# Kernel optimization log

Hardware: AMD Instinct MI355X
Metric: run time of the kernel (lower is better)

Reference implementation:

```python
import jax, jax.numpy as jnp
import numpy as np
from jax import lax

EPS = 1e-8  # numerical safety in squash sqrt (torch repo uses plain sqrt)

def squash(s, axis=-1):
    sq = jnp.sum(s * s, axis=axis, keepdims=True)
    return (sq / (1.0 + sq)) * s / jnp.sqrt(sq + EPS)

def conv2d(x, w, b, stride):
    y = lax.conv_general_dilated(x, w, (stride, stride), 'VALID',
                                 dimension_numbers=('NCHW', 'OIHW', 'NCHW'))
    return y + b[None, :, None, None]

def setup_inputs() -> dict:
    key = jax.random.key(0)
    ks = jax.random.split(key, 12)
    B = 256
    x = jax.random.normal(ks[0], (B, 1, 28, 28), dtype=jnp.float32)
    conv_w = jax.random.normal(ks[1], (256, 1, 9, 9), dtype=jnp.float32) * 0.05
    conv_b = jnp.zeros((256,), dtype=jnp.float32)
    caps1_w = jax.random.normal(ks[2], (32, 8, 256, 9, 9), dtype=jnp.float32) * 0.01
    caps1_b = jnp.zeros((32, 8), dtype=jnp.float32)
    caps2_w = jax.random.normal(ks[3], (10, 1152, 8, 16), dtype=jnp.float32)  # torch.randn
    dec_w1 = jax.random.normal(ks[4], (160, 512), dtype=jnp.float32) * 0.05
    dec_b1 = jnp.zeros((512,), dtype=jnp.float32)
    dec_w2 = jax.random.normal(ks[5], (512, 1024), dtype=jnp.float32) * 0.04
    dec_b2 = jnp.zeros((1024,), dtype=jnp.float32)
    dec_w3 = jax.random.normal(ks[6], (1024, 784), dtype=jnp.float32) * 0.03
    dec_b3 = jnp.zeros((784,), dtype=jnp.float32)
    return {"x": x, "conv_w": conv_w, "conv_b": conv_b, "caps1_w": caps1_w,
            "caps1_b": caps1_b, "caps2_w": caps2_w, "dec_w1": dec_w1,
            "dec_b1": dec_b1, "dec_w2": dec_w2, "dec_b2": dec_b2,
            "dec_w3": dec_w3, "dec_b3": dec_b3}

def reference(x, conv_w, conv_b, caps1_w, caps1_b, caps2_w,
              dec_w1, dec_b1, dec_w2, dec_b2, dec_w3, dec_b3):
    B = x.shape[0]
    # conv + relu -> [B,256,20,20]
    h = jax.nn.relu(conv2d(x, conv_w, conv_b, 1))
    # CapsLayerOne: 32 parallel convs folded into one grouped-out conv -> [B,256,6,6]
    u = conv2d(h, caps1_w.reshape(32 * 8, 256, 9, 9), caps1_b.reshape(-1), 2)
    u = u.reshape(B, 32, 8, 6, 6)                    # [B,caps,ch,h,w]
    # replicate torch cat(dim=-1).view(B,8,-1): flatten order (h, caps, w) per channel
    u = u.transpose(0, 2, 3, 1, 4).reshape(B, 8, 1152)  # [B,8,N]
    u = squash(u.transpose(0, 2, 1))                 # [B,N,8], N=1152
    # CapsLayerTwo dynamic routing
    x_hat = jnp.einsum('bni,cnio->cbno', u, caps2_w)[:, :, :, None, :]  # [10,B,N,1,16]
    b = jnp.zeros_like(x_hat)
    v = None
    for i in range(3):
        c = jax.nn.softmax(b, axis=2)
        s = jnp.sum(x_hat * c, axis=2, keepdims=True)  # [10,B,1,1,16]
        v = squash(s)
        if i != 2:
            b = b + jnp.sum(x_hat * v, axis=-1, keepdims=True)
    v = v[:, :, 0, 0, :].transpose(1, 0, 2)            # [B,10,16]
    class_scores = jnp.sqrt(jnp.sum(v * v, axis=-1) + EPS)  # [B,10]
    class_probabilities = jax.nn.softmax(class_scores, axis=-1)
    labels = jnp.argmax(class_probabilities, axis=1)
    y = jax.nn.one_hot(labels, 10, dtype=v.dtype)
    masked = (v * y[:, :, None]).reshape(B, 160)
    d = jax.nn.relu(masked @ dec_w1 + dec_b1)
    d = jax.nn.relu(d @ dec_w2 + dec_b2)
    reconstructions = jax.nn.sigmoid(d @ dec_w3 + dec_b3)  # [B,784]
    return (class_probabilities, reconstructions)
```

## Files before the change

kernel.cpp:

```cpp
#include <hip/hip_runtime.h>
#include <cstdint>
#include <cstddef>

#define EPSF 1e-8f

typedef __attribute__((ext_vector_type(8))) short bf16x8;
typedef __attribute__((ext_vector_type(4))) float f32x4;
typedef unsigned short ushort_t;

static __device__ __forceinline__ ushort_t f2bf(float f) {
  unsigned u = __builtin_bit_cast(unsigned, f);
  unsigned r = (u + 0x7FFFu + ((u >> 16) & 1u)) >> 16;
  return (ushort_t)r;
}
static __device__ __forceinline__ float bf2f(ushort_t h) {
  return __builtin_bit_cast(float, (unsigned)h << 16);
}

__global__ __launch_bounds__(256) void conv1_kernel(
    const float* __restrict__ x, const float* __restrict__ cw,
    const float* __restrict__ cb, ushort_t* __restrict__ h2x)
{
  int oy = blockIdx.x, b = blockIdx.y, ci = threadIdx.x;
  float w[81];
#pragma unroll
  for (int i = 0; i < 81; ++i) w[i] = cw[ci * 81 + i];
  float bias = cb[ci];
  float acc[20];
#pragma unroll
  for (int ox = 0; ox < 20; ++ox) acc[ox] = bias;
  const float* xb = x + (size_t)b * 784;
  for (int ky = 0; ky < 9; ++ky) {
    const float* row = xb + (oy + ky) * 28;
    float rv[28];
#pragma unroll
    for (int c = 0; c < 28; ++c) rv[c] = row[c];
#pragma unroll
    for (int kx = 0; kx < 9; ++kx) {
      float wv = w[ky * 9 + kx];
#pragma unroll
      for (int ox = 0; ox < 20; ++ox)
        acc[ox] = fmaf(rv[ox + kx], wv, acc[ox]);
    }
  }
  int cblk = ci >> 5, jj = ci & 31;
#pragma unroll
  for (int ox = 0; ox < 20; ++ox) {
    float a = fmaxf(acc[ox], 0.f);
    ushort_t hi = f2bf(a);
    ushort_t lo = f2bf(a - bf2f(hi));
    size_t o = ((size_t)(oy * 20 + ox) * 256 + b) * 512 + cblk * 64 + jj;
    h2x[o] = hi; h2x[o + 32] = lo;
  }
}

__global__ __launch_bounds__(256) void w2k_prep_kernel(
    const float* __restrict__ c1w, ushort_t* __restrict__ w2k)
{
  int co = blockIdx.x, ci = threadIdx.x;
  const float* src = c1w + ((size_t)co * 256 + ci) * 81;
  int cblk = ci >> 5, jj = ci & 31;
  for (int tap = 0; tap < 81; ++tap) {
    float v = src[tap];
    ushort_t hi = f2bf(v);
    size_t dst = ((size_t)co * 81 + tap) * 512 + cblk * 64 + jj;
    w2k[dst] = hi;
    w2k[dst + 32] = f2bf(v - bf2f(hi));
  }
}

__global__ __launch_bounds__(256, 2) void caps1_mfma_kernel(
    const ushort_t* __restrict__ h2x, const ushort_t* __restrict__ w2k,
    float* __restrict__ partial)
{
  int bid = blockIdx.x;
  int ks = bid & 3;
  int nt = (bid >> 2) & 1;
  int kt = (bid >> 3) & 1;
  int mt = (bid >> 4) & 1;
  int pos = bid >> 5;
  int ys = pos / 6, xs = pos % 6;
  int t = threadIdx.x;
  int wid = t >> 6, lane = t & 63;
  int wr = wid >> 1, wc = wid & 1;
  int lrow = lane & 15, g = lane >> 4;

  int b0 = mt * 128, n0 = nt * 128;
  int tb    = kt ? 41 : 0;
  int ntaps = kt ? 40 : 41;
  int nht   = 2 * ntaps;

  __shared__ ushort_t lds[2][2][128 * 64];

  f32x4 acc[4][4];
#pragma unroll
  for (int i = 0; i < 4; ++i)
#pragma unroll
    for (int j = 0; j < 4; ++j) acc[i][j] = (f32x4){0.f, 0.f, 0.f, 0.f};

  int c_ = (t & 7) ^ ((t >> 3) & 7);
  size_t aRowB[4], bRow81[4];
  int ldsBase[4];
#pragma unroll
  for (int i = 0; i < 4; ++i) {
    int row = i * 32 + (t >> 3);
    aRowB[i]  = (size_t)(b0 + row) * 512 + ks * 128 + c_ * 8;
    bRow81[i] = (size_t)(n0 + row) * 81;
    ldsBase[i] = (i * 32 + wid * 8) * 64;
  }

  auto stage = [&](int j, int bufi) {
    int tap = tb + (j >> 1);
    int half = j & 1;
    int ky = tap / 9, kx = tap - ky * 9;
    int pix = (2 * ys + ky) * 20 + 2 * xs + kx;
    size_t apix = (size_t)pix * 131072 + half * 64;
    int sub = ks * 128 + half * 64 + c_ * 8;
#pragma unroll
    for (int i = 0; i < 4; ++i) {
      const ushort_t* ga = h2x + apix + aRowB[i];
      const ushort_t* gb = w2k + (bRow81[i] + tap) * 512 + sub;
      __builtin_amdgcn_global_load_lds(ga, &lds[bufi][0][ldsBase[i]], 16, 0, 0);
      __builtin_amdgcn_global_load_lds(gb, &lds[bufi][1][ldsBase[i]], 16, 0, 0);
    }
  };

  bf16x8 a_h[4], a_l[4], b_h[4], b_l[4];
  auto read_frags = [&](int bufi) {
    const ushort_t* LA = &lds[bufi][0][0];
    const ushort_t* LB = &lds[bufi][1][0];
#pragma unroll
    for (int f = 0; f < 4; ++f) {
      int ra = wr * 64 + f * 16 + lrow;
      int sa = ra * 64;
      a_h[f] = *(const bf16x8*)(LA + sa + ((g)     ^ (ra & 7)) * 8);
      a_l[f] = *(const bf16x8*)(LA + sa + ((4 + g) ^ (ra & 7)) * 8);
      int rb = wc * 64 + f * 16 + lrow;
      int sb = rb * 64;
      b_h[f] = *(const bf16x8*)(LB + sb + ((g)     ^ (rb & 7)) * 8);
      b_l[f] = *(const bf16x8*)(LB + sb + ((4 + g) ^ (rb & 7)) * 8);
    }
  };

  stage(0, 0);
  stage(1, 1);
  asm volatile("s_waitcnt vmcnt(8)" ::: "memory");
  __builtin_amdgcn_sched_barrier(0);
  __builtin_amdgcn_s_barrier();

  for (int j = 0; j < nht; ++j) {
    int cur = j & 1;
    read_frags(cur);
    asm volatile("s_waitcnt lgkmcnt(0)" ::: "memory");
    __builtin_amdgcn_sched_barrier(0);
    __builtin_amdgcn_s_barrier();

    if (j + 2 < nht) stage(j + 2, cur);
    __builtin_amdgcn_sched_barrier(0);

    __builtin_amdgcn_s_setprio(1);
#pragma unroll
    for (int mf = 0; mf < 4; ++mf)
#pragma unroll
      for (int nf = 0; nf < 4; ++nf) {
        acc[mf][nf] = __builtin_amdgcn_mfma_f32_16x16x32_bf16(a_h[mf], b_h[nf], acc[mf][nf], 0, 0, 0);
        acc[mf][nf] = __builtin_amdgcn_mfma_f32_16x16x32_bf16(a_h[mf], b_l[nf], acc[mf][nf], 0, 0, 0);
        acc[mf][nf] = __builtin_amdgcn_mfma_f32_16x16x32_bf16(a_l[mf], b_h[nf], acc[mf][nf], 0, 0, 0);
      }
    __builtin_amdgcn_s_setprio(0);
    __builtin_amdgcn_sched_barrier(0);

    if (j + 2 < nht) { asm volatile("s_waitcnt vmcnt(8)" ::: "memory"); }
    else             { asm volatile("s_waitcnt vmcnt(0)" ::: "memory"); }
    __builtin_amdgcn_sched_barrier(0);
    __builtin_amdgcn_s_barrier();
  }

  float* pp = partial + (size_t)(kt * 4 + ks) * 2359296;
#pragma unroll
  for (int mf = 0; mf < 4; ++mf) {
    int m = b0 + wr * 64 + mf * 16 + g * 4;
#pragma unroll
    for (int nf = 0; nf < 4; ++nf) {
      int n = n0 + wc * 64 + nf * 16 + lrow;
#pragma unroll
      for (int r = 0; r < 4; ++r)
        pp[((size_t)(pos * 256 + m + r)) * 256 + n] = acc[mf][nf][r];
    }
  }
}

__global__ __launch_bounds__(256) void combine_kernel(
    const float* __restrict__ partial, const float* __restrict__ c1b, float* __restrict__ u)
{
  int gidx = blockIdx.x * 256 + threadIdx.x;
  int caps = gidx & 31;
  int b = (gidx >> 5) & 255;
  int pos = gidx >> 13;
  int ys = pos / 6, xs = pos % 6;
  size_t base = ((size_t)pos * 256 + b) * 256 + caps * 8;
  f32x4 s0 = {0.f, 0.f, 0.f, 0.f}, s1 = {0.f, 0.f, 0.f, 0.f};
#pragma unroll
  for (int ksp = 0; ksp < 8; ++ksp) {
    const float* pp = partial + (size_t)ksp * 2359296 + base;
    s0 += *(const f32x4*)pp;
    s1 += *(const f32x4*)(pp + 4);
  }
  const float* bp = c1b + caps * 8;
#pragma unroll
  for (int i = 0; i < 4; ++i) { s0[i] += bp[i]; s1[i] += bp[4 + i]; }
  float sq = s0[0]*s0[0] + s0[1]*s0[1] + s0[2]*s0[2] + s0[3]*s0[3]
           + s1[0]*s1[0] + s1[1]*s1[1] + s1[2]*s1[2] + s1[3]*s1[3];
  float scale = sq / ((1.f + sq) * sqrtf(sq + EPSF));
  int nvec = ys * 192 + caps * 6 + xs;
  float* up = u + ((size_t)b * 1152 + nvec) * 8;
  f32x4 o0, o1;
#pragma unroll
  for (int i = 0; i < 4; ++i) { o0[i] = s0[i] * scale; o1[i] = s1[i] * scale; }
  *(f32x4*)up = o0;
  *(f32x4*)(up + 4) = o1;
}

__global__ __launch_bounds__(320) void xhat_kernel(
    const float* __restrict__ u, const float* __restrict__ W2, float* __restrict__ xh)
{
  int np = blockIdx.x;
  int t = threadIdx.x;
  int c  = t >> 5;
  int nh = (t >> 4) & 1;
  int o  = t & 15;
  int n = np * 2 + nh;
  __shared__ float us[2][256][8];
  for (int e = t; e < 4096; e += 320) {
    int b = e >> 4;
    int nn = (e >> 3) & 1, i = e & 7;
    us[nn][b][i] = u[((size_t)b * 1152 + np * 2 + nn) * 8 + i];
  }
  __syncthreads();
  float wcol[8];
  const float* wp = W2 + (((size_t)c * 1152 + n) * 8) * 16 + o;
#pragma unroll
  for (int i = 0; i < 8; ++i) wcol[i] = wp[i * 16];
  float* xp = xh + ((size_t)(c * 256) * 1152 + n) * 16 + o;
  for (int b = 0; b < 256; ++b) {
    float s = 0.f;
#pragma unroll
    for (int i = 0; i < 8; ++i) s = fmaf(us[nh][b][i], wcol[i], s);
    xp[(size_t)b * 1152 * 16] = s;
  }
}

__global__ __launch_bounds__(256) void routing_kernel(
    const float* __restrict__ xhat, float* __restrict__ vout)
{
  int b = blockIdx.x, c = blockIdx.y, t = threadIdx.x;
  int wid = t >> 6, lane = t & 63;
  float xh[5][16];
  float bn[5] = {0, 0, 0, 0, 0};
  bool valid[5];
  const float* xp = xhat + ((size_t)(c * 256 + b)) * 1152 * 16;
#pragma unroll
  for (int j = 0; j < 5; ++j) {
    int n = t + 256 * j;
    valid[j] = (n < 1152);
    if (valid[j]) {
      const f32x4* q = (const f32x4*)(xp + (size_t)n * 16);
#pragma unroll
      for (int v4 = 0; v4 < 4; ++v4) {
        f32x4 val = q[v4];
#pragma unroll
        for (int k = 0; k < 4; ++k) xh[j][v4 * 4 + k] = val[k];
      }
    } else {
#pragma unroll
      for (int o = 0; o < 16; ++o) xh[j][o] = 0.f;
    }
  }
  __shared__ float redm[4], redz[4], reds[64], sv[16];
  float scale = 0.f;
  for (int it = 0; it < 3; ++it) {
    float m = -1e30f;
#pragma unroll
    for (int j = 0; j < 5; ++j) if (valid[j]) m = fmaxf(m, bn[j]);
    for (int d = 1; d < 64; d <<= 1) m = fmaxf(m, __shfl_xor(m, d));
    if (lane == 0) redm[wid] = m;
    __syncthreads();
    m = fmaxf(fmaxf(redm[0], redm[1]), fmaxf(redm[2], redm[3]));
    float e[5]; float z = 0.f;
#pragma unroll
    for (int j = 0; j < 5; ++j) { e[j] = valid[j] ? expf(bn[j] - m) : 0.f; z += e[j]; }
    for (int d = 1; d < 64; d <<= 1) z += __shfl_xor(z, d);
    if (lane == 0) redz[wid] = z;
    __syncthreads();
    z = redz[0] + redz[1] + redz[2] + redz[3];
    float ps[16];
#pragma unroll
    for (int o = 0; o < 16; ++o) ps[o] = 0.f;
#pragma unroll
    for (int j = 0; j < 5; ++j)
#pragma unroll
      for (int o = 0; o < 16; ++o) ps[o] = fmaf(e[j], xh[j][o], ps[o]);
#pragma unroll
    for (int o = 0; o < 16; ++o) {
      float vv = ps[o];
      for (int d = 1; d < 64; d <<= 1) vv += __shfl_xor(vv, d);
      if (lane == 0) reds[wid * 16 + o] = vv;
    }
    __syncthreads();
    if (t < 16) sv[t] = (reds[t] + reds[16 + t] + reds[32 + t] + reds[48 + t]) / z;
    __syncthreads();
    float vsc[16]; float sq = 0.f;
#pragma unroll
    for (int o = 0; o < 16; ++o) { vsc[o] = sv[o]; sq += sv[o] * sv[o]; }
    scale = sq / ((1.f + sq) * sqrtf(sq + EPSF));
    if (it < 2) {
#pragma unroll
      for (int j = 0; j < 5; ++j) if (valid[j]) {
        float dot = 0.f;
#pragma unroll
        for (int o = 0; o < 16; ++o) dot = fmaf(xh[j][o], vsc[o] * scale, dot);
        bn[j] += dot;
      }
    }
    __syncthreads();
  }
  if (t < 16) vout[((size_t)c * 256 + b) * 16 + t] = sv[t] * scale;
}

__global__ __launch_bounds__(256) void classify_kernel(
    const float* __restrict__ v, float* __restrict__ probs, float* __restrict__ masked)
{
  int b = blockIdx.x, t = threadIdx.x;
  __shared__ float sc[10], vv[160];
  int c = t >> 4, o = t & 15;
  float val = 0.f;
  if (t < 160) { val = v[((size_t)c * 256 + b) * 16 + o]; vv[t] = val; }
  float sq = val * val;
  sq += __shfl_xor(sq, 1); sq += __shfl_xor(sq, 2);
  sq += __shfl_xor(sq, 4); sq += __shfl_xor(sq, 8);
  if (t < 160 && o == 0) sc[c] = sqrtf(sq + EPSF);
  __syncthreads();
  float m = sc[0];
#pragma unroll
  for (int i = 1; i < 10; ++i) m = fmaxf(m, sc[i]);
  float ee[10]; float Z = 0.f;
#pragma unroll
  for (int i = 0; i < 10; ++i) { ee[i] = expf(sc[i] - m); Z += ee[i]; }
  float p[10];
#pragma unroll
  for (int i = 0; i < 10; ++i) p[i] = ee[i] / Z;
  int label = 0; float best = p[0];
#pragma unroll
  for (int i = 1; i < 10; ++i) if (p[i] > best) { best = p[i]; label = i; }
  if (t < 10) probs[(size_t)b * 10 + t] = p[t];
  if (t < 160) masked[(size_t)b * 160 + t] = (c == label) ? vv[t] : 0.f;
}

template <int ACT>
__global__ __launch_bounds__(256) void mlp_kernel(
    const float* __restrict__ A, const float* __restrict__ W,
    const float* __restrict__ bias, float* __restrict__ C, int N, int K)
{
  int j = blockIdx.x * 64 + (threadIdx.x & 63);
  int ty = threadIdx.x >> 6;
  int m0 = blockIdx.y * 16;
  __shared__ float As[16][33];
  float acc[4] = {0.f, 0.f, 0.f, 0.f};
  for (int k0 = 0; k0 < K; k0 += 32) {
    for (int e = threadIdx.x; e < 512; e += 256) {
      int r = e >> 5, kk = e & 31;
      As[r][kk] = A[(size_t)(m0 + r) * K + k0 + kk];
    }
    __syncthreads();
    if (j < N) {
      for (int kk = 0; kk < 32; ++kk) {
        float wv = W[(size_t)(k0 + kk) * N + j];
#pragma unroll
        for (int r = 0; r < 4; ++r) acc[r] = fmaf(As[ty + 4 * r][kk], wv, acc[r]);
      }
    }
    __syncthreads();
  }
  if (j < N) {
    float bv = bias[j];
#pragma unroll
    for (int r = 0; r < 4; ++r) {
      float xx = acc[r] + bv;
      if (ACT == 0) xx = fmaxf(xx, 0.f);
      else xx = 1.f / (1.f + expf(-xx));
      C[(size_t)(m0 + ty + 4 * r) * N + j] = xx;
    }
  }
}

extern "C" void kernel_launch(void* const* d_in, const int* in_sizes, int n_in,
                              void* d_out, int out_size, void* d_ws, size_t ws_size,
                              hipStream_t stream)
{
  const float* x   = (const float*)d_in[0];
  const float* cw  = (const float*)d_in[1];
  const float* cb  = (const float*)d_in[2];
  const float* c1w = (const float*)d_in[3];
  const float* c1b = (const float*)d_in[4];
  const float* c2w = (const float*)d_in[5];
  const float* w1  = (const float*)d_in[6];
  const float* b1  = (const float*)d_in[7];
  const float* w2  = (const float*)d_in[8];
  const float* b2  = (const float*)d_in[9];
  const float* w3  = (const float*)d_in[10];
  const float* b3  = (const float*)d_in[11];
  float* out = (float*)d_out;

  char* p = (char*)d_ws;
  float* xh = (float*)p;
  ushort_t* h2x = (ushort_t*)p; p += (size_t)52428800 * 2;
  ushort_t* w2k = (ushort_t*)p; p += (size_t)10616832 * 2;
  float* partial = (float*)p;   p += (size_t)8 * 2359296 * 4;
  float* u       = (float*)p;   p += (size_t)2359296 * 4;
  float* v       = (float*)p;   p += (size_t)40960 * 4;
  float* masked  = (float*)p;   p += (size_t)40960 * 4;
  float* a1      = (float*)p;   p += (size_t)131072 * 4;
  float* a2      = (float*)p;   p += (size_t)262144 * 4;

  hipLaunchKernelGGL(w2k_prep_kernel, dim3(256), dim3(256), 0, stream, c1w, w2k);
  hipLaunchKernelGGL(conv1_kernel, dim3(20, 256), dim3(256), 0, stream, x, cw, cb, h2x);
  hipLaunchKernelGGL(caps1_mfma_kernel, dim3(1152), dim3(256), 0, stream, h2x, w2k, partial);
  hipLaunchKernelGGL(combine_kernel, dim3(1152), dim3(256), 0, stream, partial, c1b, u);
  hipLaunchKernelGGL(xhat_kernel, dim3(576), dim3(320), 0, stream, u, c2w, xh);
  hipLaunchKernelGGL(routing_kernel, dim3(256, 10), dim3(256), 0, stream, xh, v);
  hipLaunchKernelGGL(classify_kernel, dim3(256), dim3(256), 0, stream, v, out, masked);
  hipLaunchKernelGGL(mlp_kernel<0>, dim3(8, 16), dim3(256), 0, stream, masked, w1, b1, a1, 512, 160);
  hipLaunchKernelGGL(mlp_kernel<0>, dim3(16, 16), dim3(256), 0, stream, a1, w2, b2, a2, 1024, 512);
  hipLaunchKernelGGL(mlp_kernel<1>, dim3(13, 16), dim3(256), 0, stream, a2, w3, b3, out + 2560, 784, 1024);
}
```

Baseline: 585.4 us.

## Fuse x_hat computation into routing kernel and drop the xhat intermediate buffer

The separate xhat kernel, which wrote the 10x256x1152x16 float x_hat tensor (~189MB) to global memory, is removed. The routing kernel now computes each x_hat vector in registers from u and caps2_w directly. Block indices are remapped so consecutive blocks share the same batch element across classes, improving cache reuse of u and W2. This trades a large write and read of x_hat for redundant W2 reads per batch element, which should mostly hit in L2/MALL since W2 is about 5.9MB.

```diff
diff --git a/kernel.cpp b/kernel.cpp
--- a/kernel.cpp
+++ b/kernel.cpp
@@ -221,55 +221,42 @@
   *(f32x4*)(up + 4) = o1;
 }
 
-__global__ __launch_bounds__(320) void xhat_kernel(
-    const float* __restrict__ u, const float* __restrict__ W2, float* __restrict__ xh)
-{
-  int np = blockIdx.x;
+__global__ __launch_bounds__(256) void routing_kernel(
+    const float* __restrict__ u, const float* __restrict__ W2, float* __restrict__ vout)
+{
+  int bid = blockIdx.x;
+  int c, b;
+  if (bid < 2048) { c = bid & 7; b = bid >> 3; }
+  else { int r = bid - 2048; int x = r & 7; c = 8 + (x >> 2); b = (r >> 3) * 4 + (x & 3); }
   int t = threadIdx.x;
-  int c  = t >> 5;
-  int nh = (t >> 4) & 1;
-  int o  = t & 15;
-  int n = np * 2 + nh;
-  __shared__ float us[2][256][8];
-  for (int e = t; e < 4096; e += 320) {
-    int b = e >> 4;
-    int nn = (e >> 3) & 1, i = e & 7;
-    us[nn][b][i] = u[((size_t)b * 1152 + np * 2 + nn) * 8 + i];
-  }
-  __syncthreads();
-  float wcol[8];
-  const float* wp = W2 + (((size_t)c * 1152 + n) * 8) * 16 + o;
-#pragma unroll
-  for (int i = 0; i < 8; ++i) wcol[i] = wp[i * 16];
-  float* xp = xh + ((size_t)(c * 256) * 1152 + n) * 16 + o;
-  for (int b = 0; b < 256; ++b) {
-    float s = 0.f;
-#pragma unroll
-    for (int i = 0; i < 8; ++i) s = fmaf(us[nh][b][i], wcol[i], s);
-    xp[(size_t)b * 1152 * 16] = s;
-  }
-}
-
-__global__ __launch_bounds__(256) void routing_kernel(
-    const float* __restrict__ xhat, float* __restrict__ vout)
-{
-  int b = blockIdx.x, c = blockIdx.y, t = threadIdx.x;
   int wid = t >> 6, lane = t & 63;
   float xh[5][16];
   float bn[5] = {0, 0, 0, 0, 0};
   bool valid[5];
-  const float* xp = xhat + ((size_t)(c * 256 + b)) * 1152 * 16;
+  const float* ub = u + (size_t)b * 9216;
+  const float* Wc = W2 + (size_t)c * 147456;
 #pragma unroll
   for (int j = 0; j < 5; ++j) {
     int n = t + 256 * j;
     valid[j] = (n < 1152);
     if (valid[j]) {
-      const f32x4* q = (const f32x4*)(xp + (size_t)n * 16);
-#pragma unroll
-      for (int v4 = 0; v4 < 4; ++v4) {
-        f32x4 val = q[v4];
-#pragma unroll
-        for (int k = 0; k < 4; ++k) xh[j][v4 * 4 + k] = val[k];
+      float uv[8];
+      *(f32x4*)&uv[0] = *(const f32x4*)(ub + (size_t)n * 8);
+      *(f32x4*)&uv[4] = *(const f32x4*)(ub + (size_t)n * 8 + 4);
+      const float* wn = Wc + (size_t)n * 128;
+#pragma unroll
+      for (int oc = 0; oc < 4; ++oc) {
+        f32x4 a0 = {0.f, 0.f, 0.f, 0.f}, a1 = {0.f, 0.f, 0.f, 0.f};
+#pragma unroll
+        for (int i = 0; i < 4; ++i) {
+          f32x4 w0 = *(const f32x4*)(wn + (2 * i) * 16 + oc * 4);
+          f32x4 w1 = *(const f32x4*)(wn + (2 * i + 1) * 16 + oc * 4);
+          a0 += uv[2 * i] * w0;
+          a1 += uv[2 * i + 1] * w1;
+        }
+        f32x4 s = a0 + a1;
+#pragma unroll
+        for (int k = 0; k < 4; ++k) xh[j][oc * 4 + k] = s[k];
       }
     } else {
 #pragma unroll
@@ -412,7 +399,6 @@
   float* out = (float*)d_out;
 
   char* p = (char*)d_ws;
-  float* xh = (float*)p;
   ushort_t* h2x = (ushort_t*)p; p += (size_t)52428800 * 2;
   ushort_t* w2k = (ushort_t*)p; p += (size_t)10616832 * 2;
   float* partial = (float*)p;   p += (size_t)8 * 2359296 * 4;
@@ -426,8 +412,7 @@
   hipLaunchKernelGGL(conv1_kernel, dim3(20, 256), dim3(256), 0, stream, x, cw, cb, h2x);
   hipLaunchKernelGGL(caps1_mfma_kernel, dim3(1152), dim3(256), 0, stream, h2x, w2k, partial);
   hipLaunchKernelGGL(combine_kernel, dim3(1152), dim3(256), 0, stream, partial, c1b, u);
-  hipLaunchKernelGGL(xhat_kernel, dim3(576), dim3(320), 0, stream, u, c2w, xh);
-  hipLaunchKernelGGL(routing_kernel, dim3(256, 10), dim3(256), 0, stream, xh, v);
+  hipLaunchKernelGGL(routing_kernel, dim3(2560), dim3(256), 0, stream, u, c2w, v);
   hipLaunchKernelGGL(classify_kernel, dim3(256), dim3(256), 0, stream, v, out, masked);
   hipLaunchKernelGGL(mlp_kernel<0>, dim3(8, 16), dim3(256), 0, stream, masked, w1, b1, a1, 512, 160);
   hipLaunchKernelGGL(mlp_kernel<0>, dim3(16, 16), dim3(256), 0, stream, a1, w2, b2, a2, 1024, 512);
```

Result: slower. 797.2 us (+36.2%).

## Enlarge caps1 MFMA tile to 256x256 per block and store x_hat in bf16

Applied to the files above, without the earlier changes.

The caps1 GEMM now gives each 512-thread block the full 256x256 output tile. Previously it used 128x128 tiles over 1152 blocks, so this quadruples operand reuse per global/LDS load. It also splits the fragment reads and MFMA work into two halves so LDS reads overlap compute. Separately, x_hat is written and read as bf16 instead of fp32, halving traffic between xhat_kernel and routing_kernel at some precision cost. The grid drops to 288 blocks, which may underfill the 256 CUs, and the larger accumulator set raises register pressure.

```diff
diff --git a/kernel.cpp b/kernel.cpp
--- a/kernel.cpp
+++ b/kernel.cpp
@@ -69,44 +69,41 @@
   }
 }
 
-__global__ __launch_bounds__(256, 2) void caps1_mfma_kernel(
+__global__ __launch_bounds__(512, 2) void caps1_mfma_kernel(
     const ushort_t* __restrict__ h2x, const ushort_t* __restrict__ w2k,
     float* __restrict__ partial)
 {
   int bid = blockIdx.x;
   int ks = bid & 3;
-  int nt = (bid >> 2) & 1;
-  int kt = (bid >> 3) & 1;
-  int mt = (bid >> 4) & 1;
-  int pos = bid >> 5;
+  int kt = (bid >> 2) & 1;
+  int pos = bid >> 3;
   int ys = pos / 6, xs = pos % 6;
   int t = threadIdx.x;
   int wid = t >> 6, lane = t & 63;
-  int wr = wid >> 1, wc = wid & 1;
+  int wrow = wid >> 2, wcol = wid & 3;
   int lrow = lane & 15, g = lane >> 4;
 
-  int b0 = mt * 128, n0 = nt * 128;
   int tb    = kt ? 41 : 0;
   int ntaps = kt ? 40 : 41;
   int nht   = 2 * ntaps;
 
-  __shared__ ushort_t lds[2][2][128 * 64];
-
-  f32x4 acc[4][4];
-#pragma unroll
-  for (int i = 0; i < 4; ++i)
+  __shared__ ushort_t lds[2][2][256 * 64];
+
+  f32x4 acc[8][4];
+#pragma unroll
+  for (int i = 0; i < 8; ++i)
 #pragma unroll
     for (int j = 0; j < 4; ++j) acc[i][j] = (f32x4){0.f, 0.f, 0.f, 0.f};
 
   int c_ = (t & 7) ^ ((t >> 3) & 7);
-  size_t aRowB[4], bRow81[4];
-  int ldsBase[4];
+  size_t aRowB[4], bTap[4];
+  int ldsB[4];
 #pragma unroll
   for (int i = 0; i < 4; ++i) {
-    int row = i * 32 + (t >> 3);
-    aRowB[i]  = (size_t)(b0 + row) * 512 + ks * 128 + c_ * 8;
-    bRow81[i] = (size_t)(n0 + row) * 81;
-    ldsBase[i] = (i * 32 + wid * 8) * 64;
+    int row = i * 64 + (t >> 3);
+    aRowB[i] = (size_t)row * 512 + ks * 128 + c_ * 8;
+    bTap[i]  = (size_t)row * 81 * 512 + ks * 128 + c_ * 8;
+    ldsB[i]  = i * 4096 + wid * 512;
   }
 
   auto stage = [&](int j, int bufi) {
@@ -115,31 +112,46 @@
     int ky = tap / 9, kx = tap - ky * 9;
     int pix = (2 * ys + ky) * 20 + 2 * xs + kx;
     size_t apix = (size_t)pix * 131072 + half * 64;
-    int sub = ks * 128 + half * 64 + c_ * 8;
+    size_t boff = (size_t)tap * 512 + half * 64;
 #pragma unroll
     for (int i = 0; i < 4; ++i) {
-      const ushort_t* ga = h2x + apix + aRowB[i];
-      const ushort_t* gb = w2k + (bRow81[i] + tap) * 512 + sub;
-      __builtin_amdgcn_global_load_lds(ga, &lds[bufi][0][ldsBase[i]], 16, 0, 0);
-      __builtin_amdgcn_global_load_lds(gb, &lds[bufi][1][ldsBase[i]], 16, 0, 0);
+      __builtin_amdgcn_global_load_lds(h2x + apix + aRowB[i], &lds[bufi][0][ldsB[i]], 16, 0, 0);
+      __builtin_amdgcn_global_load_lds(w2k + bTap[i] + boff,  &lds[bufi][1][ldsB[i]], 16, 0, 0);
     }
   };
 
   bf16x8 a_h[4], a_l[4], b_h[4], b_l[4];
-  auto read_frags = [&](int bufi) {
+  auto readB = [&](int bufi) {
+    const ushort_t* LB = &lds[bufi][1][0];
+#pragma unroll
+    for (int nf = 0; nf < 4; ++nf) {
+      int rb = wcol * 64 + nf * 16 + lrow;
+      int sb = rb * 64;
+      b_h[nf] = *(const bf16x8*)(LB + sb + ((g)     ^ (rb & 7)) * 8);
+      b_l[nf] = *(const bf16x8*)(LB + sb + ((4 + g) ^ (rb & 7)) * 8);
+    }
+  };
+  auto readA = [&](int bufi, int hf) {
     const ushort_t* LA = &lds[bufi][0][0];
-    const ushort_t* LB = &lds[bufi][1][0];
-#pragma unroll
-    for (int f = 0; f < 4; ++f) {
-      int ra = wr * 64 + f * 16 + lrow;
+#pragma unroll
+    for (int mf = 0; mf < 4; ++mf) {
+      int ra = wrow * 128 + (hf * 4 + mf) * 16 + lrow;
       int sa = ra * 64;
-      a_h[f] = *(const bf16x8*)(LA + sa + ((g)     ^ (ra & 7)) * 8);
-      a_l[f] = *(const bf16x8*)(LA + sa + ((4 + g) ^ (ra & 7)) * 8);
-      int rb = wc * 64 + f * 16 + lrow;
-      int sb = rb * 64;
-      b_h[f] = *(const bf16x8*)(LB + sb + ((g)     ^ (rb & 7)) * 8);
-      b_l[f] = *(const bf16x8*)(LB + sb + ((4 + g) ^ (rb & 7)) * 8);
-    }
+      a_h[mf] = *(const bf16x8*)(LA + sa + ((g)     ^ (ra & 7)) * 8);
+      a_l[mf] = *(const bf16x8*)(LA + sa + ((4 + g) ^ (ra & 7)) * 8);
+    }
+  };
+  auto mfmaH = [&](int hf) {
+    __builtin_amdgcn_s_setprio(1);
+#pragma unroll
+    for (int mf = 0; mf < 4; ++mf)
+#pragma unroll
+      for (int nf = 0; nf < 4; ++nf) {
+        acc[hf * 4 + mf][nf] = __builtin_amdgcn_mfma_f32_16x16x32_bf16(a_h[mf], b_h[nf], acc[hf * 4 + mf][nf], 0, 0, 0);
+        acc[hf * 4 + mf][nf] = __builtin_amdgcn_mfma_f32_16x16x32_bf16(a_h[mf], b_l[nf], acc[hf * 4 + mf][nf], 0, 0, 0);
+        acc[hf * 4 + mf][nf] = __builtin_amdgcn_mfma_f32_16x16x32_bf16(a_l[mf], b_h[nf], acc[hf * 4 + mf][nf], 0, 0, 0);
+      }
+    __builtin_amdgcn_s_setprio(0);
   };
 
   stage(0, 0);
@@ -150,26 +162,18 @@
 
   for (int j = 0; j < nht; ++j) {
     int cur = j & 1;
-    read_frags(cur);
+    readB(cur);
+    readA(cur, 0);
+    asm volatile("s_waitcnt lgkmcnt(0)" ::: "memory");
+    __builtin_amdgcn_sched_barrier(0);
+    mfmaH(0);
+    readA(cur, 1);
     asm volatile("s_waitcnt lgkmcnt(0)" ::: "memory");
     __builtin_amdgcn_sched_barrier(0);
     __builtin_amdgcn_s_barrier();
-
     if (j + 2 < nht) stage(j + 2, cur);
     __builtin_amdgcn_sched_barrier(0);
-
-    __builtin_amdgcn_s_setprio(1);
-#pragma unroll
-    for (int mf = 0; mf < 4; ++mf)
-#pragma unroll
-      for (int nf = 0; nf < 4; ++nf) {
-        acc[mf][nf] = __builtin_amdgcn_mfma_f32_16x16x32_bf16(a_h[mf], b_h[nf], acc[mf][nf], 0, 0, 0);
-        acc[mf][nf] = __builtin_amdgcn_mfma_f32_16x16x32_bf16(a_h[mf], b_l[nf], acc[mf][nf], 0, 0, 0);
-        acc[mf][nf] = __builtin_amdgcn_mfma_f32_16x16x32_bf16(a_l[mf], b_h[nf], acc[mf][nf], 0, 0, 0);
-      }
-    __builtin_amdgcn_s_setprio(0);
-    __builtin_amdgcn_sched_barrier(0);
-
+    mfmaH(1);
     if (j + 2 < nht) { asm volatile("s_waitcnt vmcnt(8)" ::: "memory"); }
     else             { asm volatile("s_waitcnt vmcnt(0)" ::: "memory"); }
     __builtin_amdgcn_sched_barrier(0);
@@ -178,14 +182,14 @@
 
   float* pp = partial + (size_t)(kt * 4 + ks) * 2359296;
 #pragma unroll
-  for (int mf = 0; mf < 4; ++mf) {
-    int m = b0 + wr * 64 + mf * 16 + g * 4;
+  for (int mfa = 0; mfa < 8; ++mfa) {
+    int m = wrow * 128 + mfa * 16 + g * 4;
 #pragma unroll
     for (int nf = 0; nf < 4; ++nf) {
-      int n = n0 + wc * 64 + nf * 16 + lrow;
+      int n = wcol * 64 + nf * 16 + lrow;
 #pragma unroll
       for (int r = 0; r < 4; ++r)
-        pp[((size_t)(pos * 256 + m + r)) * 256 + n] = acc[mf][nf][r];
+        pp[((size_t)(pos * 256 + m + r)) * 256 + n] = acc[mfa][nf][r];
     }
   }
 }
@@ -222,7 +226,7 @@
 }
 
 __global__ __launch_bounds__(320) void xhat_kernel(
-    const float* __restrict__ u, const float* __restrict__ W2, float* __restrict__ xh)
+    const float* __restrict__ u, const float* __restrict__ W2, ushort_t* __restrict__ xh)
 {
   int np = blockIdx.x;
   int t = threadIdx.x;
@@ -241,36 +245,35 @@
   const float* wp = W2 + (((size_t)c * 1152 + n) * 8) * 16 + o;
 #pragma unroll
   for (int i = 0; i < 8; ++i) wcol[i] = wp[i * 16];
-  float* xp = xh + ((size_t)(c * 256) * 1152 + n) * 16 + o;
+  ushort_t* xp = xh + ((size_t)(c * 256) * 1152 + n) * 16 + o;
   for (int b = 0; b < 256; ++b) {
     float s = 0.f;
 #pragma unroll
     for (int i = 0; i < 8; ++i) s = fmaf(us[nh][b][i], wcol[i], s);
-    xp[(size_t)b * 1152 * 16] = s;
+    xp[(size_t)b * 18432] = f2bf(s);
   }
 }
 
 __global__ __launch_bounds__(256) void routing_kernel(
-    const float* __restrict__ xhat, float* __restrict__ vout)
+    const ushort_t* __restrict__ xhat, float* __restrict__ vout)
 {
   int b = blockIdx.x, c = blockIdx.y, t = threadIdx.x;
   int wid = t >> 6, lane = t & 63;
   float xh[5][16];
   float bn[5] = {0, 0, 0, 0, 0};
   bool valid[5];
-  const float* xp = xhat + ((size_t)(c * 256 + b)) * 1152 * 16;
+  const ushort_t* xp = xhat + ((size_t)(c * 256 + b)) * 1152 * 16;
 #pragma unroll
   for (int j = 0; j < 5; ++j) {
     int n = t + 256 * j;
     valid[j] = (n < 1152);
     if (valid[j]) {
-      const f32x4* q = (const f32x4*)(xp + (size_t)n * 16);
-#pragma unroll
-      for (int v4 = 0; v4 < 4; ++v4) {
-        f32x4 val = q[v4];
-#pragma unroll
-        for (int k = 0; k < 4; ++k) xh[j][v4 * 4 + k] = val[k];
-      }
+      const bf16x8* q = (const bf16x8*)(xp + (size_t)n * 16);
+      bf16x8 v0 = q[0], v1 = q[1];
+#pragma unroll
+      for (int k = 0; k < 8; ++k) xh[j][k] = bf2f((ushort_t)v0[k]);
+#pragma unroll
+      for (int k = 0; k < 8; ++k) xh[j][8 + k] = bf2f((ushort_t)v1[k]);
     } else {
 #pragma unroll
       for (int o = 0; o < 16; ++o) xh[j][o] = 0.f;
@@ -412,7 +415,7 @@
   float* out = (float*)d_out;
 
   char* p = (char*)d_ws;
-  float* xh = (float*)p;
+  ushort_t* xh = (ushort_t*)p;
   ushort_t* h2x = (ushort_t*)p; p += (size_t)52428800 * 2;
   ushort_t* w2k = (ushort_t*)p; p += (size_t)10616832 * 2;
   float* partial = (float*)p;   p += (size_t)8 * 2359296 * 4;
@@ -424,7 +427,7 @@
 
   hipLaunchKernelGGL(w2k_prep_kernel, dim3(256), dim3(256), 0, stream, c1w, w2k);
   hipLaunchKernelGGL(conv1_kernel, dim3(20, 256), dim3(256), 0, stream, x, cw, cb, h2x);
-  hipLaunchKernelGGL(caps1_mfma_kernel, dim3(1152), dim3(256), 0, stream, h2x, w2k, partial);
+  hipLaunchKernelGGL(caps1_mfma_kernel, dim3(288), dim3(512), 0, stream, h2x, w2k, partial);
   hipLaunchKernelGGL(combine_kernel, dim3(1152), dim3(256), 0, stream, partial, c1b, u);
   hipLaunchKernelGGL(xhat_kernel, dim3(576), dim3(320), 0, stream, u, c2w, xh);
   hipLaunchKernelGGL(routing_kernel, dim3(256, 10), dim3(256), 0, stream, xh, v);
```

Measured after the change: 658.3 us. 1.12x slower.
